# Performance work log

Hardware: AMD Instinct MI355X
Metric: run time of the kernel (lower is better)

The kernel has to match this reference:

```python
import jax, jax.numpy as jnp
import numpy as np

N_HEAD = 16
D_K = 128
D_MODEL = N_HEAD * D_K  # 2048


def setup_inputs() -> dict:
    key = jax.random.key(0)
    ks = jax.random.split(key, 12)
    bs, q_len, kv_len = 32, 16, 2048
    scale = 1.0 / np.sqrt(D_MODEL)
    inp = {
        "x": jax.random.normal(ks[0], (bs, q_len, D_MODEL), jnp.float32),
        "k_cache": jax.random.normal(ks[1], (bs, kv_len, D_MODEL), jnp.float32),
        "v_cache": jax.random.normal(ks[2], (bs, kv_len, D_MODEL), jnp.float32),
        "mask": jnp.ones((bs, q_len, kv_len), jnp.int32),
        "Wq": jax.random.normal(ks[3], (D_MODEL, D_MODEL), jnp.float32) * scale,
        "bq": jnp.zeros((D_MODEL,), jnp.float32),
        "Wk": jax.random.normal(ks[4], (D_MODEL, D_MODEL), jnp.float32) * scale,
        "bk": jnp.zeros((D_MODEL,), jnp.float32),
        "Wv": jax.random.normal(ks[5], (D_MODEL, D_MODEL), jnp.float32) * scale,
        "bv": jnp.zeros((D_MODEL,), jnp.float32),
        "Wo": jax.random.normal(ks[6], (D_MODEL, D_MODEL), jnp.float32) * scale,
        "bo": jnp.zeros((D_MODEL,), jnp.float32),
    }
    return inp


def reference(x, k_cache, v_cache, mask, Wq, bq, Wk, bk, Wv, bv, Wo, bo):
    bs, q_len, d_model = x.shape
    # QKV projections (nn.Linear => x @ W.T + b)
    q = x @ Wq.T + bq
    k = x @ Wk.T + bk
    v = x @ Wv.T + bv
    # KV-cache slice write at the last q_len positions
    k_cache = k_cache.at[:, -q_len:, :].set(k)
    v_cache = v_cache.at[:, -q_len:, :].set(v)
    # split heads: [b, s, h, dk] -> [b, h, s, dk]
    qh = q.reshape(bs, q_len, N_HEAD, D_K).transpose(0, 2, 1, 3)
    kh = k_cache.reshape(bs, -1, N_HEAD, D_K).transpose(0, 2, 1, 3)
    vh = v_cache.reshape(bs, -1, N_HEAD, D_K).transpose(0, 2, 1, 3)
    # scaled dot-product attention with mask broadcast over heads
    scores = jnp.einsum("bhqd,bhkd->bhqk", qh, kh) / np.sqrt(D_K)
    scores = jnp.where(mask[:, None, :, :] == 0, jnp.float32(-1e9), scores)
    attn = jax.nn.softmax(scores, axis=-1)
    out = jnp.einsum("bhqk,bhkd->bhqd", attn, vh)
    out = out.transpose(0, 2, 1, 3).reshape(bs, q_len, d_model)
    # output projection (dropout is identity at inference)
    out = out @ Wo.T + bo
    return (out, k_cache, v_cache)
```

## Files before the change

kernel.cpp:

```cpp
#include <hip/hip_runtime.h>
#include <hip/hip_bf16.h>

#define BS 32
#define QL 16
#define KV 2048
#define NH 16
#define DK 128
#define DM 2048
#define MROWS (BS*QL)
#define KCA 4
#define AROWS (KV/KCA)
#define KCB 2
#define BROWS (KV/KCB)
#define SPLICE (KV-QL)

#define SCALE 0.08838834764831845f
#define LOG2E 1.4426950408889634f

typedef __bf16 bf16x8 __attribute__((ext_vector_type(8)));
typedef float f32x4 __attribute__((ext_vector_type(4)));
typedef unsigned short us8 __attribute__((ext_vector_type(8)));
typedef unsigned short us4 __attribute__((ext_vector_type(4)));

__device__ inline unsigned short f2bf(float f){
    unsigned u = __builtin_bit_cast(unsigned, f);
    u += 0x7fffu + ((u >> 16) & 1u);
    return (unsigned short)(u >> 16);
}
__device__ inline float bf2f(unsigned short u){
    unsigned x = ((unsigned)u) << 16;
    return __builtin_bit_cast(float, x);
}

__global__ __launch_bounds__(256) void gemm_bt(
    const float* __restrict__ A0p, const float* __restrict__ A1p,
    const float* __restrict__ W0, const float* __restrict__ W1, const float* __restrict__ W2,
    const float* __restrict__ b0, const float* __restrict__ b1, const float* __restrict__ b2,
    float* __restrict__ C0, float* __restrict__ C1, float* __restrict__ C2,
    int spliceMask)
{
    int z = blockIdx.z;
    const float* W    = (z==0)?W0:(z==1)?W1:W2;
    const float* bias = (z==0)?b0:(z==1)?b1:b2;
    float*       C    = (z==0)?C0:(z==1)?C1:C2;
    int spl = (spliceMask >> z) & 1;

    const int K = DM, N = DM;
    int mBase = blockIdx.x * 64, nBase = blockIdx.y * 64;

    __shared__ __align__(16) unsigned short As[64*40];
    __shared__ __align__(16) unsigned short Bs[64*40];

    int t = threadIdx.x;
    int wv = t >> 6, lane = t & 63;
    int row = t >> 2, seg = (t & 3) * 8;
    int g = lane >> 4, c = lane & 15;

    f32x4 acc[4] = {{0,0,0,0},{0,0,0,0},{0,0,0,0},{0,0,0,0}};

    for (int k0 = 0; k0 < K; k0 += 32) {
        __syncthreads();
        {
            size_t off = (size_t)(mBase + row) * K + k0 + seg;
            float4 a0 = *(const float4*)(A0p + off), a1 = *(const float4*)(A0p + off + 4);
            if (A1p) {
                float4 c0 = *(const float4*)(A1p + off), c1 = *(const float4*)(A1p + off + 4);
                a0.x+=c0.x; a0.y+=c0.y; a0.z+=c0.z; a0.w+=c0.w;
                a1.x+=c1.x; a1.y+=c1.y; a1.z+=c1.z; a1.w+=c1.w;
            }
            us8 av = { f2bf(a0.x), f2bf(a0.y), f2bf(a0.z), f2bf(a0.w),
                       f2bf(a1.x), f2bf(a1.y), f2bf(a1.z), f2bf(a1.w) };
            *(us8*)&As[row*40 + seg] = av;
        }
        {
            const float* wp = W + (size_t)(nBase + row) * K + k0 + seg;
            float4 w0v = *(const float4*)wp, w1v = *(const float4*)(wp + 4);
            us8 wv8 = { f2bf(w0v.x), f2bf(w0v.y), f2bf(w0v.z), f2bf(w0v.w),
                        f2bf(w1v.x), f2bf(w1v.y), f2bf(w1v.z), f2bf(w1v.w) };
            *(us8*)&Bs[row*40 + seg] = wv8;
        }
        __syncthreads();

        bf16x8 af = __builtin_bit_cast(bf16x8, *(us8*)&As[(wv*16 + c)*40 + g*8]);
        #pragma unroll
        for (int j = 0; j < 4; j++) {
            bf16x8 bf = __builtin_bit_cast(bf16x8, *(us8*)&Bs[(j*16 + c)*40 + g*8]);
            acc[j] = __builtin_amdgcn_mfma_f32_16x16x32_bf16(af, bf, acc[j], 0, 0, 0);
        }
    }

    #pragma unroll
    for (int j = 0; j < 4; j++) {
        int n = nBase + j*16 + c;
        float bb = bias[n];
        #pragma unroll
        for (int r = 0; r < 4; r++) {
            int m = mBase + wv*16 + g*4 + r;
            size_t rowoff = spl ? ((size_t)(m >> 4) * KV + SPLICE + (m & 15)) * (size_t)N
                                : (size_t)m * (size_t)N;
            C[rowoff + n] = acc[j][r] + bb;
        }
    }
}

__global__ __launch_bounds__(256) void kcopy_p(
    const float* __restrict__ qws, const float* __restrict__ kcache,
    const int* __restrict__ mask,
    float* __restrict__ kout, __hip_bfloat16* __restrict__ Pbuf,
    float* __restrict__ statsL)
{
    int h = blockIdx.x, b = blockIdx.y, kc = blockIdx.z;
    int t = threadIdx.x, wv = t >> 6, lane = t & 63;
    int g = lane >> 4, c = lane & 15;
    size_t bKV = (size_t)b * KV;
    size_t bh  = (size_t)b * NH + h;
    unsigned short* P = (unsigned short*)Pbuf;

    __shared__ float smL[4][16];

    bf16x8 af[4];
    {
        const float* qp = qws + (size_t)(b*QL + c) * DM + h*DK + g*8;
        #pragma unroll
        for (int ks = 0; ks < 4; ks++) {
            float4 q0 = *(const float4*)(qp + ks*32);
            float4 q1 = *(const float4*)(qp + ks*32 + 4);
            us8 qv = { f2bf(q0.x*SCALE), f2bf(q0.y*SCALE), f2bf(q0.z*SCALE), f2bf(q0.w*SCALE),
                       f2bf(q1.x*SCALE), f2bf(q1.y*SCALE), f2bf(q1.z*SCALE), f2bf(q1.w*SCALE) };
            af[ks] = __builtin_bit_cast(bf16x8, qv);
        }
    }

    float lloc[4] = {0.f,0.f,0.f,0.f};

    for (int i = 0; i < 8; i++) {
        int n0 = kc*AROWS + (i*4 + wv)*16;
        int krow = n0 + c;
        bool spl = (n0 >= SPLICE);
        const float* src = (spl ? kout : kcache) + (bKV + krow)*DM + h*DK + g*8;

        float4 kvv[8];
        #pragma unroll
        for (int ks = 0; ks < 4; ks++) {
            kvv[2*ks]   = *(const float4*)(src + ks*32);
            kvv[2*ks+1] = *(const float4*)(src + ks*32 + 4);
        }
        if (!spl) {
            float* dst = kout + (bKV + krow)*DM + h*DK + g*8;
            #pragma unroll
            for (int ks = 0; ks < 4; ks++) {
                *(float4*)(dst + ks*32)     = kvv[2*ks];
                *(float4*)(dst + ks*32 + 4) = kvv[2*ks+1];
            }
        }
        f32x4 sc = {0,0,0,0};
        #pragma unroll
        for (int ks = 0; ks < 4; ks++) {
            float4 k0 = kvv[2*ks], k1 = kvv[2*ks+1];
            us8 kb = { f2bf(k0.x), f2bf(k0.y), f2bf(k0.z), f2bf(k0.w),
                       f2bf(k1.x), f2bf(k1.y), f2bf(k1.z), f2bf(k1.w) };
            sc = __builtin_amdgcn_mfma_f32_16x16x32_bf16(af[ks],
                    __builtin_bit_cast(bf16x8, kb), sc, 0, 0, 0);
        }
        const int* mrow = mask + (size_t)b * QL * KV + krow;
        us4 pv4;
        #pragma unroll
        for (int r = 0; r < 4; r++) {
            int q = g*4 + r;
            float p = (mrow[(size_t)q * KV] == 0) ? 0.f : exp2f(sc[r]*LOG2E);
            pv4[r] = f2bf(p);
            lloc[r] += p;
        }
        *(us4*)(void*)&P[(bh*KV + krow)*QL + g*4] = pv4;
    }

    #pragma unroll
    for (int r = 0; r < 4; r++) {
        float l = lloc[r];
        #pragma unroll
        for (int mm = 1; mm < 16; mm <<= 1) l += __shfl_xor(l, mm);
        if (c == 0) smL[wv][g*4 + r] = l;
    }
    __syncthreads();
    if (t < 16) {
        float L = 0.f;
        #pragma unroll
        for (int w = 0; w < 4; w++) L += smL[w][t];
        statsL[(bh*KCA + kc)*QL + t] = L;
    }
}

__global__ __launch_bounds__(256) void vcopy_pv(
    const float* __restrict__ vcache, const __hip_bfloat16* __restrict__ Pbuf,
    const float* __restrict__ statsL,
    float* __restrict__ vout, float* __restrict__ awsP)
{
    int hd = blockIdx.x; int h = hd >> 1, half = hd & 1;
    int b = blockIdx.y, kc = blockIdx.z;
    int t = threadIdx.x;
    size_t bKV = (size_t)b * KV;
    size_t bh  = (size_t)b * NH + h;
    const unsigned short* P = (const unsigned short*)Pbuf;

    __shared__ float smLinv[16];
    __shared__ __align__(16) unsigned short Vl[64*72];
    __shared__ __align__(16) float Pl[16*68];

    if (t < 16) {
        float L = 0.f;
        #pragma unroll
        for (int c4 = 0; c4 < KCA; c4++)
            L += statsL[(bh*KCA + c4)*QL + t];
        smLinv[t] = 1.0f / L;
    }
    __syncthreads();

    int q = t >> 4, dc = t & 15;
    int srow = t >> 2;
    int vseg = (t & 3) * 16;
    int pq0  = (t & 3) * 4;

    float O[4] = {0.f,0.f,0.f,0.f};

    for (int kt = 0; kt < 16; kt++) {
        int k0 = kc*BROWS + kt*64;
        __syncthreads();
        {
            int krow = k0 + srow;
            us4 sv = *(const us4*)(const void*)&P[(bh*KV + krow)*QL + pq0];
            #pragma unroll
            for (int j = 0; j < 4; j++)
                Pl[(pq0+j)*68 + srow] = bf2f(sv[j]);
        }
        {
            int vrow = k0 + srow;
            bool cpy = (vrow < SPLICE);
            const float* src = (cpy ? vcache : vout) + (bKV + vrow)*DM + h*DK + half*64 + vseg;
            float4 v0 = *(const float4*)(src);
            float4 v1 = *(const float4*)(src + 4);
            float4 v2 = *(const float4*)(src + 8);
            float4 v3 = *(const float4*)(src + 12);
            if (cpy) {
                float* dst = vout + (bKV + vrow)*DM + h*DK + half*64 + vseg;
                *(float4*)(dst)      = v0;
                *(float4*)(dst + 4)  = v1;
                *(float4*)(dst + 8)  = v2;
                *(float4*)(dst + 12) = v3;
            }
            us8 p0 = { f2bf(v0.x), f2bf(v0.y), f2bf(v0.z), f2bf(v0.w),
                       f2bf(v1.x), f2bf(v1.y), f2bf(v1.z), f2bf(v1.w) };
            us8 p1 = { f2bf(v2.x), f2bf(v2.y), f2bf(v2.z), f2bf(v2.w),
                       f2bf(v3.x), f2bf(v3.y), f2bf(v3.z), f2bf(v3.w) };
            *(us8*)&Vl[srow*72 + vseg]     = p0;
            *(us8*)&Vl[srow*72 + vseg + 8] = p1;
        }
        __syncthreads();
        #pragma unroll
        for (int kk0 = 0; kk0 < 64; kk0 += 4) {
            float4 pv = *(const float4*)&Pl[q*68 + kk0];
            #pragma unroll
            for (int j = 0; j < 4; j++) {
                us4 vb = *(const us4*)(const void*)&Vl[(kk0+j)*72 + dc*4];
                float pj = pv[j];
                O[0] += pj*bf2f(vb[0]); O[1] += pj*bf2f(vb[1]);
                O[2] += pj*bf2f(vb[2]); O[3] += pj*bf2f(vb[3]);
            }
        }
    }

    float inv = smLinv[q];
    float* op = awsP + (size_t)kc * MROWS * DM
              + (size_t)(b*QL + q)*DM + h*DK + half*64 + dc*4;
    float4 ov = {O[0]*inv, O[1]*inv, O[2]*inv, O[3]*inv};
    *(float4*)op = ov;
}

extern "C" void kernel_launch(void* const* d_in, const int* in_sizes, int n_in,
                              void* d_out, int out_size, void* d_ws, size_t ws_size,
                              hipStream_t stream)
{
    (void)in_sizes; (void)n_in; (void)out_size; (void)ws_size;

    const float* x      = (const float*)d_in[0];
    const float* kcache = (const float*)d_in[1];
    const float* vcache = (const float*)d_in[2];
    const int*   mask   = (const int*)  d_in[3];
    const float* Wq     = (const float*)d_in[4];
    const float* bq     = (const float*)d_in[5];
    const float* Wk     = (const float*)d_in[6];
    const float* bk     = (const float*)d_in[7];
    const float* Wv     = (const float*)d_in[8];
    const float* bv     = (const float*)d_in[9];
    const float* Wo     = (const float*)d_in[10];
    const float* bo     = (const float*)d_in[11];

    float* out  = (float*)d_out;
    float* kout = out  + (size_t)MROWS * DM;
    float* vout = kout + (size_t)BS * KV * DM;

    float* qws    = (float*)d_ws;
    float* aws0   = qws  + (size_t)MROWS * DM;
    float* aws1   = aws0 + (size_t)MROWS * DM;
    float* statsL = aws1 + (size_t)MROWS * DM;
    __hip_bfloat16* Pbuf = (__hip_bfloat16*)(statsL + (size_t)BS * NH * KCA * QL);

    dim3 gq(MROWS/64, DM/64, 3);
    gemm_bt<<<gq, 256, 0, stream>>>(x, nullptr,
                                    Wq, Wk, Wv, bq, bk, bv,
                                    qws, kout, vout, 0b110);

    dim3 ga(NH, BS, KCA);
    kcopy_p<<<ga, 256, 0, stream>>>(qws, kcache, mask, kout, Pbuf, statsL);

    dim3 gb(NH*2, BS, KCB);
    vcopy_pv<<<gb, 256, 0, stream>>>(vcache, Pbuf, statsL, vout, aws0);

    dim3 go(MROWS/64, DM/64, 1);
    gemm_bt<<<go, 256, 0, stream>>>(aws0, aws1,
                                    Wo, Wo, Wo, bo, bo, bo,
                                    out, out, out, 0);
}
```

Before: 634.7 us.

## Fuse K and V cache passes into one split-K attention kernel with MFMA PV

Merges the QK/softmax kernel and the V-copy/PV kernel into one kernel. Each block now copies both its K and V slices, computes unnormalised probabilities, and runs the PV product on MFMA through a per-wave LDS tile, all without writing P to global memory. Per-wave partial outputs are reduced in shared memory and stored as bf16 partials, and a small combine kernel sums the split-K chunks and normalises before the output GEMM. This removes the P round-trip and the scalar FMA PV loop, at the cost of an extra launch, bf16 rounding of partial outputs, and more LDS per block.

```diff
diff --git a/kernel.cpp b/kernel.cpp
--- a/kernel.cpp
+++ b/kernel.cpp
@@ -10,8 +10,6 @@
 #define MROWS (BS*QL)
 #define KCA 4
 #define AROWS (KV/KCA)
-#define KCB 2
-#define BROWS (KV/KCB)
 #define SPLICE (KV-QL)
 
 #define SCALE 0.08838834764831845f
@@ -103,19 +101,22 @@
     }
 }
 
-__global__ __launch_bounds__(256) void kcopy_p(
+__global__ __launch_bounds__(256) void fused_kv_attn(
     const float* __restrict__ qws, const float* __restrict__ kcache,
-    const int* __restrict__ mask,
-    float* __restrict__ kout, __hip_bfloat16* __restrict__ Pbuf,
-    float* __restrict__ statsL)
+    const float* __restrict__ vcache, const int* __restrict__ mask,
+    float* __restrict__ kout, float* __restrict__ vout,
+    __hip_bfloat16* __restrict__ Obuf, float* __restrict__ Lbuf)
 {
     int h = blockIdx.x, b = blockIdx.y, kc = blockIdx.z;
     int t = threadIdx.x, wv = t >> 6, lane = t & 63;
     int g = lane >> 4, c = lane & 15;
     size_t bKV = (size_t)b * KV;
     size_t bh  = (size_t)b * NH + h;
-    unsigned short* P = (unsigned short*)Pbuf;
-
+    unsigned short* Ob = (unsigned short*)Obuf;
+
+    __shared__ __align__(16) unsigned char smem[4*16*132*4];
+    unsigned short* Vl = (unsigned short*)smem;
+    float* redf = (float*)smem;
     __shared__ float smL[4][16];
 
     bf16x8 af[4];
@@ -131,26 +132,31 @@
         }
     }
 
-    float lloc[4] = {0.f,0.f,0.f,0.f};
+    f32x4 Oacc[8];
+    #pragma unroll
+    for (int nt = 0; nt < 8; nt++) Oacc[nt] = (f32x4){0,0,0,0};
+    float lacc = 0.f;
+
+    unsigned short* Vw = Vl + wv*2304;
 
     for (int i = 0; i < 8; i++) {
         int n0 = kc*AROWS + (i*4 + wv)*16;
+        bool spl = (n0 >= SPLICE);
+
         int krow = n0 + c;
-        bool spl = (n0 >= SPLICE);
-        const float* src = (spl ? kout : kcache) + (bKV + krow)*DM + h*DK + g*8;
-
+        const float* ksrc = (spl ? kout : kcache) + (bKV + krow)*DM + h*DK + g*8;
         float4 kvv[8];
         #pragma unroll
         for (int ks = 0; ks < 4; ks++) {
-            kvv[2*ks]   = *(const float4*)(src + ks*32);
-            kvv[2*ks+1] = *(const float4*)(src + ks*32 + 4);
+            kvv[2*ks]   = *(const float4*)(ksrc + ks*32);
+            kvv[2*ks+1] = *(const float4*)(ksrc + ks*32 + 4);
         }
         if (!spl) {
-            float* dst = kout + (bKV + krow)*DM + h*DK + g*8;
+            float* kdst = kout + (bKV + krow)*DM + h*DK + g*8;
             #pragma unroll
             for (int ks = 0; ks < 4; ks++) {
-                *(float4*)(dst + ks*32)     = kvv[2*ks];
-                *(float4*)(dst + ks*32 + 4) = kvv[2*ks+1];
+                *(float4*)(kdst + ks*32)     = kvv[2*ks];
+                *(float4*)(kdst + ks*32 + 4) = kvv[2*ks+1];
             }
         }
         f32x4 sc = {0,0,0,0};
@@ -159,120 +165,103 @@
             float4 k0 = kvv[2*ks], k1 = kvv[2*ks+1];
             us8 kb = { f2bf(k0.x), f2bf(k0.y), f2bf(k0.z), f2bf(k0.w),
                        f2bf(k1.x), f2bf(k1.y), f2bf(k1.z), f2bf(k1.w) };
-            sc = __builtin_amdgcn_mfma_f32_16x16x32_bf16(af[ks],
-                    __builtin_bit_cast(bf16x8, kb), sc, 0, 0, 0);
-        }
-        const int* mrow = mask + (size_t)b * QL * KV + krow;
-        us4 pv4;
+            sc = __builtin_amdgcn_mfma_f32_16x16x32_bf16(
+                    __builtin_bit_cast(bf16x8, kb), af[ks], sc, 0, 0, 0);
+        }
+
+        const int4 mv = *(const int4*)(mask + ((size_t)b*QL + c)*KV + n0 + g*4);
+        int mi[4] = {mv.x, mv.y, mv.z, mv.w};
+        float p[4];
         #pragma unroll
         for (int r = 0; r < 4; r++) {
-            int q = g*4 + r;
-            float p = (mrow[(size_t)q * KV] == 0) ? 0.f : exp2f(sc[r]*LOG2E);
-            pv4[r] = f2bf(p);
-            lloc[r] += p;
-        }
-        *(us4*)(void*)&P[(bh*KV + krow)*QL + g*4] = pv4;
-    }
-
-    #pragma unroll
-    for (int r = 0; r < 4; r++) {
-        float l = lloc[r];
-        #pragma unroll
-        for (int mm = 1; mm < 16; mm <<= 1) l += __shfl_xor(l, mm);
-        if (c == 0) smL[wv][g*4 + r] = l;
-    }
+            p[r] = mi[r] ? exp2f(sc[r]*LOG2E) : 0.f;
+            lacc += p[r];
+        }
+        us8 pa = { f2bf(p[0]), f2bf(p[1]), f2bf(p[2]), f2bf(p[3]), 0, 0, 0, 0 };
+        bf16x8 paf = __builtin_bit_cast(bf16x8, pa);
+
+        #pragma unroll
+        for (int f = 0; f < 8; f++) {
+            int k  = (f & 1)*8 + (lane >> 3);
+            int d0 = ((lane & 7)*4) + (f >> 1)*32;
+            size_t off = (bKV + n0 + k)*DM + h*DK + d0;
+            const float* vs = (spl ? vout : vcache) + off;
+            float4 v = *(const float4*)vs;
+            if (!spl) *(float4*)(vout + off) = v;
+            int e = (d0 >> 4)*288 + (k >> 2)*72 + (k & 3)*16 + (d0 & 15);
+            us4 bv4 = { f2bf(v.x), f2bf(v.y), f2bf(v.z), f2bf(v.w) };
+            *(us4*)&Vw[e] = bv4;
+        }
+
+        #pragma unroll
+        for (int nt = 0; nt < 8; nt++) {
+            const unsigned short* vb = Vw + nt*288 + g*72 + c;
+            us8 b8 = { vb[0], vb[16], vb[32], vb[48], 0, 0, 0, 0 };
+            Oacc[nt] = __builtin_amdgcn_mfma_f32_16x16x32_bf16(
+                          paf, __builtin_bit_cast(bf16x8, b8), Oacc[nt], 0, 0, 0);
+        }
+    }
+
+    lacc += __shfl_xor(lacc, 16);
+    lacc += __shfl_xor(lacc, 32);
+    if (lane < 16) smL[wv][lane] = lacc;
+
     __syncthreads();
-    if (t < 16) {
-        float L = 0.f;
-        #pragma unroll
-        for (int w = 0; w < 4; w++) L += smL[w][t];
-        statsL[(bh*KCA + kc)*QL + t] = L;
-    }
-}
-
-__global__ __launch_bounds__(256) void vcopy_pv(
-    const float* __restrict__ vcache, const __hip_bfloat16* __restrict__ Pbuf,
-    const float* __restrict__ statsL,
-    float* __restrict__ vout, float* __restrict__ awsP)
+
+    #pragma unroll
+    for (int nt = 0; nt < 8; nt++)
+        #pragma unroll
+        for (int r = 0; r < 4; r++)
+            redf[wv*2112 + (g*4 + r)*132 + c + nt*16] = Oacc[nt][r];
+    __syncthreads();
+
+    {
+        int q = t >> 4, d0 = (t & 15)*8;
+        float s[8] = {0,0,0,0,0,0,0,0};
+        #pragma unroll
+        for (int w = 0; w < 4; w++) {
+            float4 x0 = *(const float4*)&redf[w*2112 + q*132 + d0];
+            float4 x1 = *(const float4*)&redf[w*2112 + q*132 + d0 + 4];
+            s[0]+=x0.x; s[1]+=x0.y; s[2]+=x0.z; s[3]+=x0.w;
+            s[4]+=x1.x; s[5]+=x1.y; s[6]+=x1.z; s[7]+=x1.w;
+        }
+        us8 o = { f2bf(s[0]), f2bf(s[1]), f2bf(s[2]), f2bf(s[3]),
+                  f2bf(s[4]), f2bf(s[5]), f2bf(s[6]), f2bf(s[7]) };
+        *(us8*)(void*)&Ob[(((size_t)kc*(BS*NH) + bh)*QL + q)*DK + d0] = o;
+        if (t < 16)
+            Lbuf[(bh*KCA + kc)*QL + t] = smL[0][t] + smL[1][t] + smL[2][t] + smL[3][t];
+    }
+}
+
+__global__ __launch_bounds__(256) void attn_combine(
+    const __hip_bfloat16* __restrict__ Obuf, const float* __restrict__ Lbuf,
+    float* __restrict__ aws)
 {
-    int hd = blockIdx.x; int h = hd >> 1, half = hd & 1;
-    int b = blockIdx.y, kc = blockIdx.z;
-    int t = threadIdx.x;
-    size_t bKV = (size_t)b * KV;
-    size_t bh  = (size_t)b * NH + h;
-    const unsigned short* P = (const unsigned short*)Pbuf;
-
-    __shared__ float smLinv[16];
-    __shared__ __align__(16) unsigned short Vl[64*72];
-    __shared__ __align__(16) float Pl[16*68];
-
-    if (t < 16) {
-        float L = 0.f;
-        #pragma unroll
-        for (int c4 = 0; c4 < KCA; c4++)
-            L += statsL[(bh*KCA + c4)*QL + t];
-        smLinv[t] = 1.0f / L;
-    }
-    __syncthreads();
-
-    int q = t >> 4, dc = t & 15;
-    int srow = t >> 2;
-    int vseg = (t & 3) * 16;
-    int pq0  = (t & 3) * 4;
-
-    float O[4] = {0.f,0.f,0.f,0.f};
-
-    for (int kt = 0; kt < 16; kt++) {
-        int k0 = kc*BROWS + kt*64;
-        __syncthreads();
-        {
-            int krow = k0 + srow;
-            us4 sv = *(const us4*)(const void*)&P[(bh*KV + krow)*QL + pq0];
-            #pragma unroll
-            for (int j = 0; j < 4; j++)
-                Pl[(pq0+j)*68 + srow] = bf2f(sv[j]);
-        }
-        {
-            int vrow = k0 + srow;
-            bool cpy = (vrow < SPLICE);
-            const float* src = (cpy ? vcache : vout) + (bKV + vrow)*DM + h*DK + half*64 + vseg;
-            float4 v0 = *(const float4*)(src);
-            float4 v1 = *(const float4*)(src + 4);
-            float4 v2 = *(const float4*)(src + 8);
-            float4 v3 = *(const float4*)(src + 12);
-            if (cpy) {
-                float* dst = vout + (bKV + vrow)*DM + h*DK + half*64 + vseg;
-                *(float4*)(dst)      = v0;
-                *(float4*)(dst + 4)  = v1;
-                *(float4*)(dst + 8)  = v2;
-                *(float4*)(dst + 12) = v3;
-            }
-            us8 p0 = { f2bf(v0.x), f2bf(v0.y), f2bf(v0.z), f2bf(v0.w),
-                       f2bf(v1.x), f2bf(v1.y), f2bf(v1.z), f2bf(v1.w) };
-            us8 p1 = { f2bf(v2.x), f2bf(v2.y), f2bf(v2.z), f2bf(v2.w),
-                       f2bf(v3.x), f2bf(v3.y), f2bf(v3.z), f2bf(v3.w) };
-            *(us8*)&Vl[srow*72 + vseg]     = p0;
-            *(us8*)&Vl[srow*72 + vseg + 8] = p1;
-        }
-        __syncthreads();
-        #pragma unroll
-        for (int kk0 = 0; kk0 < 64; kk0 += 4) {
-            float4 pv = *(const float4*)&Pl[q*68 + kk0];
-            #pragma unroll
-            for (int j = 0; j < 4; j++) {
-                us4 vb = *(const us4*)(const void*)&Vl[(kk0+j)*72 + dc*4];
-                float pj = pv[j];
-                O[0] += pj*bf2f(vb[0]); O[1] += pj*bf2f(vb[1]);
-                O[2] += pj*bf2f(vb[2]); O[3] += pj*bf2f(vb[3]);
-            }
-        }
-    }
-
-    float inv = smLinv[q];
-    float* op = awsP + (size_t)kc * MROWS * DM
-              + (size_t)(b*QL + q)*DM + h*DK + half*64 + dc*4;
-    float4 ov = {O[0]*inv, O[1]*inv, O[2]*inv, O[3]*inv};
-    *(float4*)op = ov;
+    int idx8 = blockIdx.x * 256 + threadIdx.x;
+    int m = idx8 >> 8;
+    int col = (idx8 & 255) * 8;
+    int b = m >> 4, q = m & 15;
+    int h = col >> 7, d0 = col & 127;
+    size_t bh = (size_t)b * NH + h;
+    const unsigned short* Ob = (const unsigned short*)Obuf;
+
+    float L = 0.f;
+    #pragma unroll
+    for (int kc = 0; kc < KCA; kc++) L += Lbuf[(bh*KCA + kc)*QL + q];
+    float inv = 1.0f / L;
+
+    float s[8] = {0,0,0,0,0,0,0,0};
+    #pragma unroll
+    for (int kc = 0; kc < KCA; kc++) {
+        us8 o = *(const us8*)(const void*)&Ob[(((size_t)kc*(BS*NH) + bh)*QL + q)*DK + d0];
+        #pragma unroll
+        for (int j = 0; j < 8; j++) s[j] += bf2f(o[j]);
+    }
+    float* op = aws + (size_t)m * DM + col;
+    float4 o0 = {s[0]*inv, s[1]*inv, s[2]*inv, s[3]*inv};
+    float4 o1 = {s[4]*inv, s[5]*inv, s[6]*inv, s[7]*inv};
+    *(float4*)op = o0;
+    *(float4*)(op + 4) = o1;
 }
 
 extern "C" void kernel_launch(void* const* d_in, const int* in_sizes, int n_in,
@@ -298,25 +287,24 @@
     float* kout = out  + (size_t)MROWS * DM;
     float* vout = kout + (size_t)BS * KV * DM;
 
-    float* qws    = (float*)d_ws;
-    float* aws0   = qws  + (size_t)MROWS * DM;
-    float* aws1   = aws0 + (size_t)MROWS * DM;
-    float* statsL = aws1 + (size_t)MROWS * DM;
-    __hip_bfloat16* Pbuf = (__hip_bfloat16*)(statsL + (size_t)BS * NH * KCA * QL);
+    float* qws  = (float*)d_ws;
+    float* aws  = qws + (size_t)MROWS * DM;
+    float* Lbuf = aws + (size_t)MROWS * DM;
+    __hip_bfloat16* Obuf = (__hip_bfloat16*)(Lbuf + (size_t)BS*NH*KCA*QL);
 
     dim3 gq(MROWS/64, DM/64, 3);
     gemm_bt<<<gq, 256, 0, stream>>>(x, nullptr,
                                     Wq, Wk, Wv, bq, bk, bv,
                                     qws, kout, vout, 0b110);
 
-    dim3 ga(NH, BS, KCA);
-    kcopy_p<<<ga, 256, 0, stream>>>(qws, kcache, mask, kout, Pbuf, statsL);
-
-    dim3 gb(NH*2, BS, KCB);
-    vcopy_pv<<<gb, 256, 0, stream>>>(vcache, Pbuf, statsL, vout, aws0);
+    dim3 gf(NH, BS, KCA);
+    fused_kv_attn<<<gf, 256, 0, stream>>>(qws, kcache, vcache, mask,
+                                          kout, vout, Obuf, Lbuf);
+
+    attn_combine<<<512, 256, 0, stream>>>(Obuf, Lbuf, aws);
 
     dim3 go(MROWS/64, DM/64, 1);
-    gemm_bt<<<go, 256, 0, stream>>>(aws0, aws1,
+    gemm_bt<<<go, 256, 0, stream>>>(aws, nullptr,
                                     Wo, Wo, Wo, bo, bo, bo,
                                     out, out, out, 0);
 }
```

Result: faster. 568.0 us (-10.5%).
